# Performance work log

Hardware: AMD Instinct MI355X
Metric: run time of the kernel (lower is better)

## Reference

```python
import jax, jax.numpy as jnp
import numpy as np

D_MODEL = 512
DK = 4
DV = 8
HIDD = 10
HEAD = D_MODEL // DV  # 64
LN_EPS = 1e-5


def setup_inputs() -> dict:
    key = jax.random.key(0)
    ks = jax.random.split(key, 10)
    B, S, Se = 8, 512, 512
    u = jax.random.uniform  # torch.rand initializer for attention weights
    n = jax.random.normal
    return {
        "x": n(ks[0], (B, S, D_MODEL), jnp.float32),
        "x_enc": n(ks[1], (B, Se, D_MODEL), jnp.float32),
        "WqM": u(ks[2], (D_MODEL, HEAD * DK), jnp.float32),
        "WkM": u(ks[3], (D_MODEL, HEAD * DK), jnp.float32),
        "WvM": u(ks[4], (D_MODEL, HEAD * DV), jnp.float32),
        "ln_g": jnp.ones((D_MODEL,), jnp.float32),
        "ln_b": jnp.zeros((D_MODEL,), jnp.float32),
        "fc1_w": n(ks[5], (HIDD, D_MODEL), jnp.float32) * (1.0 / np.sqrt(D_MODEL)),
        "fc1_b": jnp.zeros((HIDD,), jnp.float32),
        "fc2_w": n(ks[6], (D_MODEL, HIDD), jnp.float32) * (1.0 / np.sqrt(HIDD)),
        "fc2_b": jnp.zeros((D_MODEL,), jnp.float32),
    }


def _attention(Xq, Xkv, WqM, WkM, WvM, causal_mul_mask):
    # NOTE: cross-attention in the source also uses WqM/WkM/WvM (Wq/Wk/Wv unused).
    B, Sq, _ = Xq.shape
    Sk = Xkv.shape[1]
    Q = (Xq @ WqM).reshape(B, Sq, HEAD, DK)
    K = (Xkv @ WkM).reshape(B, Sk, HEAD, DK)
    V = (Xkv @ WvM).reshape(B, Sk, HEAD, DV)
    score = jnp.einsum('bqhd,bkhd->bhqk', Q, K) / np.sqrt(DK).astype(np.float32)
    if causal_mul_mask:
        # Faithful quirk: multiplicative tril mask on scores (NOT additive -inf).
        score = score * jnp.tril(jnp.ones((Sq, Sk), score.dtype))
    w = jax.nn.softmax(score, axis=-1)
    out = jnp.einsum('bhqk,bkhd->bqhd', w, V)
    return out.reshape(B, Sq, HEAD * DV)  # HEAD*DV == d_model


def _layernorm(x, g, b):
    mu = jnp.mean(x, axis=-1, keepdims=True)
    var = jnp.mean(jnp.square(x - mu), axis=-1, keepdims=True)
    return (x - mu) * jax.lax.rsqrt(var + LN_EPS) * g + b


def reference(x, x_enc, WqM, WkM, WvM, ln_g, ln_b, fc1_w, fc1_b, fc2_w, fc2_b):
    fx = _attention(x, x, WqM, WkM, WvM, causal_mul_mask=True)
    fx = _attention(fx, x_enc, WqM, WkM, WvM, causal_mul_mask=False)
    y = _layernorm(x + fx, ln_g, ln_b)
    h = jax.nn.relu(y @ fc1_w.T + fc1_b)
    return h @ fc2_w.T + fc2_b
```

## Files before the change

### kernel.cpp

```cpp
#include <hip/hip_runtime.h>
#include <math.h>

#define D_MODEL 512
#define BATCH 8
#define SEQ 512
#define HEAD 64
#define DK 4
#define DV 8
#define HIDD 10

#define MR 32
#define KC 32
#define NC 256

__global__ __launch_bounds__(256) void proj_kernel(
    const float* __restrict__ xq, const float* __restrict__ xkv,
    const float* __restrict__ Wq, const float* __restrict__ Wk,
    const float* __restrict__ Wv,
    float* __restrict__ Q2, float* __restrict__ K2, float* __restrict__ V2)
{
    __shared__ float xt[KC * MR];
    __shared__ float wt[KC * NC];

    const int t  = threadIdx.x;
    const int bj = blockIdx.x & 3;
    const int br = blockIdx.x >> 2;
    const int r0 = br * MR;

    const float* X; const float* W; int ldw; int c0;
    if (bj == 0)      { X = xq;  W = Wq; ldw = 256; c0 = 0;   }
    else if (bj == 1) { X = xkv; W = Wk; ldw = 256; c0 = 0;   }
    else if (bj == 2) { X = xkv; W = Wv; ldw = 512; c0 = 0;   }
    else              { X = xkv; W = Wv; ldw = 512; c0 = 256; }

    const int rg = t >> 6;
    const int cq = t & 63;
    const int rs = t & 31;
    const int kq = t >> 5;

    float4 acc[8];
#pragma unroll
    for (int r = 0; r < 8; ++r) acc[r] = make_float4(0.f, 0.f, 0.f, 0.f);

    for (int kc = 0; kc < D_MODEL; kc += KC) {
        const float4 xa = *(const float4*)(X + (long)(r0 + rs) * D_MODEL + kc + kq * 4);
        xt[(kq * 4 + 0) * MR + rs] = xa.x;
        xt[(kq * 4 + 1) * MR + rs] = xa.y;
        xt[(kq * 4 + 2) * MR + rs] = xa.z;
        xt[(kq * 4 + 3) * MR + rs] = xa.w;

#pragma unroll
        for (int i = 0; i < 8; ++i) {
            const int row = i * 4 + rg;
            *(float4*)(wt + row * NC + cq * 4) =
                *(const float4*)(W + (long)(kc + row) * ldw + c0 + cq * 4);
        }
        __syncthreads();

#pragma unroll 4
        for (int k = 0; k < KC; ++k) {
            const float4 w4 = *(const float4*)(wt + k * NC + cq * 4);
            const float4 x0 = *(const float4*)(xt + k * MR + rg * 8);
            const float4 x1 = *(const float4*)(xt + k * MR + rg * 8 + 4);
            const float xr[8] = {x0.x, x0.y, x0.z, x0.w, x1.x, x1.y, x1.z, x1.w};
#pragma unroll
            for (int r = 0; r < 8; ++r) {
                acc[r].x = fmaf(xr[r], w4.x, acc[r].x);
                acc[r].y = fmaf(xr[r], w4.y, acc[r].y);
                acc[r].z = fmaf(xr[r], w4.z, acc[r].z);
                acc[r].w = fmaf(xr[r], w4.w, acc[r].w);
            }
        }
        __syncthreads();
    }

    const int b = r0 >> 9;
    const int sb = (r0 & 511) + rg * 8;
    if (bj <= 1) {
        float* dst = (bj == 0) ? Q2 : K2;
#pragma unroll
        for (int r = 0; r < 8; ++r)
            *(float4*)(dst + (((long)b * HEAD + cq) * SEQ + sb + r) * 4) = acc[r];
    } else {
        const int col = c0 + cq * 4;
        const int h = col >> 3;
        const int off = col & 7;
#pragma unroll
        for (int r = 0; r < 8; ++r)
            *(float4*)(V2 + (((long)b * HEAD + h) * SEQ + sb + r) * 8 + off) = acc[r];
    }
}

__global__ __launch_bounds__(256) void attn_kernel(
    const float* __restrict__ Q2, const float* __restrict__ K2,
    const float* __restrict__ V2, float* __restrict__ O, int causal)
{
    extern __shared__ float smem[];
    float* Kl = smem;
    float* Vl = smem + SEQ * DK;
    float* cs = Vl + SEQ * DV;

    const int t = threadIdx.x;
    const int bh = blockIdx.x >> 1;
    const int qhalf = blockIdx.x & 1;
    const int b = bh >> 6;
    const int h = bh & 63;

    const float4* Ks = (const float4*)(K2 + (long)bh * SEQ * DK);
    ((float4*)Kl)[t]       = Ks[t];
    ((float4*)Kl)[t + 256] = Ks[t + 256];
    const float4* Vs = (const float4*)(V2 + (long)bh * SEQ * DV);
#pragma unroll
    for (int i = 0; i < 4; ++i)
        ((float4*)Vl)[t + i * 256] = Vs[t + i * 256];
    __syncthreads();

    if (causal) {
        const int ch = t >> 3, d = t & 7;
        float s16 = 0.f;
#pragma unroll
        for (int i = 0; i < 16; ++i) s16 += Vl[(ch * 16 + i) * 8 + d];
        cs[ch * 8 + d] = s16;
        __syncthreads();
        if (t < 8) {
            cs[256 + t] = 0.f;
            float run = 0.f;
            for (int c2 = 31; c2 >= 0; --c2) {
                run += cs[c2 * 8 + t];
                cs[c2 * 8 + t] = run;
            }
        }
        __syncthreads();
    }

    const int q = qhalf * 256 + t;
    const float4 qv = *(const float4*)(Q2 + ((long)bh * SEQ + q) * 4);
    const float q0 = qv.x * 0.5f, q1 = qv.y * 0.5f;
    const float q2 = qv.z * 0.5f, q3 = qv.w * 0.5f;

    const int bound = causal ? q : (SEQ - 1);

    float m = -INFINITY, l = 0.f;
    float a0=0.f,a1=0.f,a2=0.f,a3=0.f,a4=0.f,a5=0.f,a6=0.f,a7=0.f;

    int s0 = 0;
    for (; s0 + 8 <= bound + 1; s0 += 8) {
        float sc[8];
#pragma unroll
        for (int i = 0; i < 8; ++i) {
            const float4 k4 = *(const float4*)(Kl + (s0 + i) * 4);
            sc[i] = fmaf(q0, k4.x, fmaf(q1, k4.y, fmaf(q2, k4.z, q3 * k4.w)));
        }
        float gm = fmaxf(fmaxf(fmaxf(sc[0], sc[1]), fmaxf(sc[2], sc[3])),
                         fmaxf(fmaxf(sc[4], sc[5]), fmaxf(sc[6], sc[7])));
        if (gm > m) {
            float scale = __expf(m - gm);
            l *= scale;
            a0*=scale; a1*=scale; a2*=scale; a3*=scale;
            a4*=scale; a5*=scale; a6*=scale; a7*=scale;
            m = gm;
        }
#pragma unroll
        for (int i = 0; i < 8; ++i) {
            float p = __expf(sc[i] - m);
            l += p;
            const float4 v0 = *(const float4*)(Vl + (s0 + i) * 8);
            const float4 v1 = *(const float4*)(Vl + (s0 + i) * 8 + 4);
            a0 = fmaf(p, v0.x, a0); a1 = fmaf(p, v0.y, a1);
            a2 = fmaf(p, v0.z, a2); a3 = fmaf(p, v0.w, a3);
            a4 = fmaf(p, v1.x, a4); a5 = fmaf(p, v1.y, a5);
            a6 = fmaf(p, v1.z, a6); a7 = fmaf(p, v1.w, a7);
        }
    }
    for (int s = s0; s <= bound; ++s) {
        const float4 k4 = *(const float4*)(Kl + s * 4);
        float sc = fmaf(q0, k4.x, fmaf(q1, k4.y, fmaf(q2, k4.z, q3 * k4.w)));
        if (sc > m) {
            float scale = __expf(m - sc);
            l *= scale;
            a0*=scale; a1*=scale; a2*=scale; a3*=scale;
            a4*=scale; a5*=scale; a6*=scale; a7*=scale;
            m = sc;
        }
        float p = __expf(sc - m);
        l += p;
        const float4 v0 = *(const float4*)(Vl + s * 8);
        const float4 v1 = *(const float4*)(Vl + s * 8 + 4);
        a0 = fmaf(p, v0.x, a0); a1 = fmaf(p, v0.y, a1);
        a2 = fmaf(p, v0.z, a2); a3 = fmaf(p, v0.w, a3);
        a4 = fmaf(p, v1.x, a4); a5 = fmaf(p, v1.y, a5);
        a6 = fmaf(p, v1.z, a6); a7 = fmaf(p, v1.w, a7);
    }

    if (causal && q < SEQ - 1) {
        float M = fmaxf(m, 0.f);
        float scale = __expf(m - M);
        float pm = __expf(-M);
        l = l * scale + pm * (float)(SEQ - 1 - q);
        int nq = q + 1;
        int cq2 = nq >> 4;
        float sv[8];
#pragma unroll
        for (int d = 0; d < 8; ++d) sv[d] = cs[(cq2 + 1) * 8 + d];
        for (int s = nq; s < (cq2 + 1) * 16; ++s) {
            const float4 v0 = *(const float4*)(Vl + s * 8);
            const float4 v1 = *(const float4*)(Vl + s * 8 + 4);
            sv[0]+=v0.x; sv[1]+=v0.y; sv[2]+=v0.z; sv[3]+=v0.w;
            sv[4]+=v1.x; sv[5]+=v1.y; sv[6]+=v1.z; sv[7]+=v1.w;
        }
        a0 = a0*scale + pm*sv[0]; a1 = a1*scale + pm*sv[1];
        a2 = a2*scale + pm*sv[2]; a3 = a3*scale + pm*sv[3];
        a4 = a4*scale + pm*sv[4]; a5 = a5*scale + pm*sv[5];
        a6 = a6*scale + pm*sv[6]; a7 = a7*scale + pm*sv[7];
    }

    float inv = 1.0f / l;
    const long obase = (long)b * SEQ * 512 + (long)q * 512 + h * DV;
    *(float4*)(O + obase)     = make_float4(a0*inv, a1*inv, a2*inv, a3*inv);
    *(float4*)(O + obase + 4) = make_float4(a4*inv, a5*inv, a6*inv, a7*inv);
}

__global__ __launch_bounds__(256) void ln_mlp_kernel(
    const float* __restrict__ x, const float* __restrict__ fx,
    const float* __restrict__ g, const float* __restrict__ beta,
    const float* __restrict__ w1, const float* __restrict__ b1,
    const float* __restrict__ w2, const float* __restrict__ b2,
    float* __restrict__ out)
{
    const int t = threadIdx.x;
    const int lane = t & 63;
    const int row = blockIdx.x * 4 + (t >> 6);
    const long base = (long)row * D_MODEL;
    const int e0 = lane * 8;

    const float4 xa = *(const float4*)(x + base + e0);
    const float4 xb = *(const float4*)(x + base + e0 + 4);
    const float4 fa = *(const float4*)(fx + base + e0);
    const float4 fb = *(const float4*)(fx + base + e0 + 4);
    float z[8] = {xa.x+fa.x, xa.y+fa.y, xa.z+fa.z, xa.w+fa.w,
                  xb.x+fb.x, xb.y+fb.y, xb.z+fb.z, xb.w+fb.w};

    float sum = 0.f;
#pragma unroll
    for (int j = 0; j < 8; ++j) sum += z[j];
#pragma unroll
    for (int o = 32; o > 0; o >>= 1) sum += __shfl_xor(sum, o);
    float mu = sum * (1.0f / 512.0f);

    float d[8], ss = 0.f;
#pragma unroll
    for (int j = 0; j < 8; ++j) { d[j] = z[j] - mu; ss += d[j] * d[j]; }
#pragma unroll
    for (int o = 32; o > 0; o >>= 1) ss += __shfl_xor(ss, o);
    float rs = rsqrtf(ss * (1.0f / 512.0f) + 1e-5f);

    const float4 ga = *(const float4*)(g + e0);
    const float4 gb = *(const float4*)(g + e0 + 4);
    const float4 ba = *(const float4*)(beta + e0);
    const float4 bb = *(const float4*)(beta + e0 + 4);
    const float gg[8] = {ga.x,ga.y,ga.z,ga.w,gb.x,gb.y,gb.z,gb.w};
    const float bt[8] = {ba.x,ba.y,ba.z,ba.w,bb.x,bb.y,bb.z,bb.w};
    float y[8];
#pragma unroll
    for (int j = 0; j < 8; ++j) y[j] = d[j] * rs * gg[j] + bt[j];

    float part[HIDD];
#pragma unroll
    for (int i = 0; i < HIDD; ++i) {
        const float4 wa = *(const float4*)(w1 + i * 512 + e0);
        const float4 wb = *(const float4*)(w1 + i * 512 + e0 + 4);
        part[i] = y[0]*wa.x + y[1]*wa.y + y[2]*wa.z + y[3]*wa.w
                + y[4]*wb.x + y[5]*wb.y + y[6]*wb.z + y[7]*wb.w;
    }
#pragma unroll
    for (int i = 0; i < HIDD; ++i)
#pragma unroll
        for (int o = 32; o > 0; o >>= 1) part[i] += __shfl_xor(part[i], o);

    float hv[HIDD];
#pragma unroll
    for (int i = 0; i < HIDD; ++i) hv[i] = fmaxf(part[i] + b1[i], 0.f);

    float o8[8];
#pragma unroll
    for (int j = 0; j < 8; ++j) o8[j] = b2[e0 + j];
#pragma unroll
    for (int i = 0; i < HIDD; ++i)
#pragma unroll
        for (int j = 0; j < 8; ++j)
            o8[j] = fmaf(hv[i], w2[(long)(e0 + j) * 10 + i], o8[j]);

    *(float4*)(out + base + e0)     = make_float4(o8[0], o8[1], o8[2], o8[3]);
    *(float4*)(out + base + e0 + 4) = make_float4(o8[4], o8[5], o8[6], o8[7]);
}

extern "C" void kernel_launch(void* const* d_in, const int* in_sizes, int n_in,
                              void* d_out, int out_size, void* d_ws, size_t ws_size,
                              hipStream_t stream) {
    (void)in_sizes; (void)n_in; (void)out_size; (void)ws_size;
    const float* x    = (const float*)d_in[0];
    const float* xenc = (const float*)d_in[1];
    const float* Wq   = (const float*)d_in[2];
    const float* Wk   = (const float*)d_in[3];
    const float* Wv   = (const float*)d_in[4];
    const float* ln_g = (const float*)d_in[5];
    const float* ln_b = (const float*)d_in[6];
    const float* w1   = (const float*)d_in[7];
    const float* b1   = (const float*)d_in[8];
    const float* w2   = (const float*)d_in[9];
    const float* b2   = (const float*)d_in[10];
    float* out = (float*)d_out;

    float* ws = (float*)d_ws;
    float* Q2 = ws;
    float* K2 = Q2 + 1048576;
    float* V2 = K2 + 1048576;
    float* A  = V2 + 2097152;

    const int nrows = BATCH * SEQ;
    const size_t lds_cross  = (size_t)(SEQ * DK + SEQ * DV) * 4;
    const size_t lds_causal = lds_cross + (size_t)(33 * DV) * 4;
    const int proj_grid = (nrows / MR) * 4;

    proj_kernel<<<dim3(proj_grid), 256, 0, stream>>>(x, x, Wq, Wk, Wv, Q2, K2, V2);
    attn_kernel<<<dim3(BATCH * HEAD * 2), 256, lds_causal, stream>>>(Q2, K2, V2, A, 1);

    proj_kernel<<<dim3(proj_grid), 256, 0, stream>>>(A, xenc, Wq, Wk, Wv, Q2, K2, V2);
    attn_kernel<<<dim3(BATCH * HEAD * 2), 256, lds_cross, stream>>>(Q2, K2, V2, A, 0);

    ln_mlp_kernel<<<dim3(nrows / 4), 256, 0, stream>>>(x, A, ln_g, ln_b,
                                                       w1, b1, w2, b2, out);
}
```

Measured before the change: 340.8 us.

## Enlarge projection register tile and process two queries per attention thread

The projection GEMM now uses 64-row tiles with an 8x8 register tile per thread, which raises arithmetic intensity per LDS load. The attention kernel handles two interleaved queries per thread, launches one block per (batch, head) instead of two, and turns the causal flag into a template parameter. Interleaving the queries also balances the causal work within each block. The risks are higher register pressure and half as many attention blocks, which lowers occupancy and parallelism.

```diff
diff --git a/kernel.cpp b/kernel.cpp
--- a/kernel.cpp
+++ b/kernel.cpp
@@ -9,7 +9,7 @@
 #define DV 8
 #define HIDD 10
 
-#define MR 32
+#define MR 64
 #define KC 32
 #define NC 256
 
@@ -33,22 +33,32 @@
     else if (bj == 2) { X = xkv; W = Wv; ldw = 512; c0 = 0;   }
     else              { X = xkv; W = Wv; ldw = 512; c0 = 256; }
 
+    const int ct = t & 31;
+    const int rt = t >> 5;
+    const int rs = t & 63;
+    const int kx = t >> 6;
     const int rg = t >> 6;
     const int cq = t & 63;
-    const int rs = t & 31;
-    const int kq = t >> 5;
-
-    float4 acc[8];
-#pragma unroll
-    for (int r = 0; r < 8; ++r) acc[r] = make_float4(0.f, 0.f, 0.f, 0.f);
+
+    float acc[8][8];
+#pragma unroll
+    for (int r = 0; r < 8; ++r)
+#pragma unroll
+        for (int c = 0; c < 8; ++c) acc[r][c] = 0.f;
 
     for (int kc = 0; kc < D_MODEL; kc += KC) {
-        const float4 xa = *(const float4*)(X + (long)(r0 + rs) * D_MODEL + kc + kq * 4);
-        xt[(kq * 4 + 0) * MR + rs] = xa.x;
-        xt[(kq * 4 + 1) * MR + rs] = xa.y;
-        xt[(kq * 4 + 2) * MR + rs] = xa.z;
-        xt[(kq * 4 + 3) * MR + rs] = xa.w;
-
+        {
+            const float4 xa = *(const float4*)(X + (long)(r0 + rs) * D_MODEL + kc + kx * 8);
+            const float4 xb = *(const float4*)(X + (long)(r0 + rs) * D_MODEL + kc + kx * 8 + 4);
+            xt[(kx * 8 + 0) * MR + rs] = xa.x;
+            xt[(kx * 8 + 1) * MR + rs] = xa.y;
+            xt[(kx * 8 + 2) * MR + rs] = xa.z;
+            xt[(kx * 8 + 3) * MR + rs] = xa.w;
+            xt[(kx * 8 + 4) * MR + rs] = xb.x;
+            xt[(kx * 8 + 5) * MR + rs] = xb.y;
+            xt[(kx * 8 + 6) * MR + rs] = xb.z;
+            xt[(kx * 8 + 7) * MR + rs] = xb.w;
+        }
 #pragma unroll
         for (int i = 0; i < 8; ++i) {
             const int row = i * 4 + rg;
@@ -57,43 +67,52 @@
         }
         __syncthreads();
 
-#pragma unroll 4
+#pragma unroll 2
         for (int k = 0; k < KC; ++k) {
-            const float4 w4 = *(const float4*)(wt + k * NC + cq * 4);
-            const float4 x0 = *(const float4*)(xt + k * MR + rg * 8);
-            const float4 x1 = *(const float4*)(xt + k * MR + rg * 8 + 4);
+            const float4 w0 = *(const float4*)(wt + k * NC + ct * 8);
+            const float4 w1 = *(const float4*)(wt + k * NC + ct * 8 + 4);
+            const float4 x0 = *(const float4*)(xt + k * MR + rt * 8);
+            const float4 x1 = *(const float4*)(xt + k * MR + rt * 8 + 4);
             const float xr[8] = {x0.x, x0.y, x0.z, x0.w, x1.x, x1.y, x1.z, x1.w};
-#pragma unroll
-            for (int r = 0; r < 8; ++r) {
-                acc[r].x = fmaf(xr[r], w4.x, acc[r].x);
-                acc[r].y = fmaf(xr[r], w4.y, acc[r].y);
-                acc[r].z = fmaf(xr[r], w4.z, acc[r].z);
-                acc[r].w = fmaf(xr[r], w4.w, acc[r].w);
-            }
+            const float wc[8] = {w0.x, w0.y, w0.z, w0.w, w1.x, w1.y, w1.z, w1.w};
+#pragma unroll
+            for (int r = 0; r < 8; ++r)
+#pragma unroll
+                for (int c = 0; c < 8; ++c)
+                    acc[r][c] = fmaf(xr[r], wc[c], acc[r][c]);
         }
         __syncthreads();
     }
 
-    const int b = r0 >> 9;
-    const int sb = (r0 & 511) + rg * 8;
+    const int b  = r0 >> 9;
+    const int sb = (r0 & 511) + rt * 8;
     if (bj <= 1) {
         float* dst = (bj == 0) ? Q2 : K2;
-#pragma unroll
-        for (int r = 0; r < 8; ++r)
-            *(float4*)(dst + (((long)b * HEAD + cq) * SEQ + sb + r) * 4) = acc[r];
+        const long h0 = (long)b * HEAD + ct * 2;
+#pragma unroll
+        for (int r = 0; r < 8; ++r) {
+            *(float4*)(dst + (h0 * SEQ + sb + r) * 4) =
+                make_float4(acc[r][0], acc[r][1], acc[r][2], acc[r][3]);
+            *(float4*)(dst + ((h0 + 1) * SEQ + sb + r) * 4) =
+                make_float4(acc[r][4], acc[r][5], acc[r][6], acc[r][7]);
+        }
     } else {
-        const int col = c0 + cq * 4;
-        const int h = col >> 3;
-        const int off = col & 7;
-#pragma unroll
-        for (int r = 0; r < 8; ++r)
-            *(float4*)(V2 + (((long)b * HEAD + h) * SEQ + sb + r) * 8 + off) = acc[r];
+        const int h = (c0 >> 3) + ct;
+        const long vb = ((long)b * HEAD + h) * SEQ;
+#pragma unroll
+        for (int r = 0; r < 8; ++r) {
+            *(float4*)(V2 + (vb + sb + r) * 8) =
+                make_float4(acc[r][0], acc[r][1], acc[r][2], acc[r][3]);
+            *(float4*)(V2 + (vb + sb + r) * 8 + 4) =
+                make_float4(acc[r][4], acc[r][5], acc[r][6], acc[r][7]);
+        }
     }
 }
 
+template <int CAUSAL>
 __global__ __launch_bounds__(256) void attn_kernel(
     const float* __restrict__ Q2, const float* __restrict__ K2,
-    const float* __restrict__ V2, float* __restrict__ O, int causal)
+    const float* __restrict__ V2, float* __restrict__ O)
 {
     extern __shared__ float smem[];
     float* Kl = smem;
@@ -101,8 +120,7 @@
     float* cs = Vl + SEQ * DV;
 
     const int t = threadIdx.x;
-    const int bh = blockIdx.x >> 1;
-    const int qhalf = blockIdx.x & 1;
+    const int bh = blockIdx.x;
     const int b = bh >> 6;
     const int h = bh & 63;
 
@@ -115,7 +133,7 @@
         ((float4*)Vl)[t + i * 256] = Vs[t + i * 256];
     __syncthreads();
 
-    if (causal) {
+    if (CAUSAL) {
         const int ch = t >> 3, d = t & 7;
         float s16 = 0.f;
 #pragma unroll
@@ -133,72 +151,102 @@
         __syncthreads();
     }
 
-    const int q = qhalf * 256 + t;
-    const float4 qv = *(const float4*)(Q2 + ((long)bh * SEQ + q) * 4);
-    const float q0 = qv.x * 0.5f, q1 = qv.y * 0.5f;
-    const float q2 = qv.z * 0.5f, q3 = qv.w * 0.5f;
-
-    const int bound = causal ? q : (SEQ - 1);
-
-    float m = -INFINITY, l = 0.f;
-    float a0=0.f,a1=0.f,a2=0.f,a3=0.f,a4=0.f,a5=0.f,a6=0.f,a7=0.f;
+    const int q0 = 2 * t, q1 = 2 * t + 1;
+    const float4 qa = *(const float4*)(Q2 + ((long)bh * SEQ + q0) * 4);
+    const float4 qb = *(const float4*)(Q2 + ((long)bh * SEQ + q1) * 4);
+    const float qa0 = qa.x*0.5f, qa1 = qa.y*0.5f, qa2 = qa.z*0.5f, qa3 = qa.w*0.5f;
+    const float qb0 = qb.x*0.5f, qb1 = qb.y*0.5f, qb2 = qb.z*0.5f, qb3 = qb.w*0.5f;
+
+    const int bound = CAUSAL ? q1 : (SEQ - 1);
+
+    float m0 = -INFINITY, l0 = 0.f, m1 = -INFINITY, l1 = 0.f;
+    float A0[8], A1[8];
+#pragma unroll
+    for (int d = 0; d < 8; ++d) { A0[d] = 0.f; A1[d] = 0.f; }
 
     int s0 = 0;
     for (; s0 + 8 <= bound + 1; s0 += 8) {
-        float sc[8];
+        float sa[8], sb[8];
 #pragma unroll
         for (int i = 0; i < 8; ++i) {
             const float4 k4 = *(const float4*)(Kl + (s0 + i) * 4);
-            sc[i] = fmaf(q0, k4.x, fmaf(q1, k4.y, fmaf(q2, k4.z, q3 * k4.w)));
-        }
-        float gm = fmaxf(fmaxf(fmaxf(sc[0], sc[1]), fmaxf(sc[2], sc[3])),
-                         fmaxf(fmaxf(sc[4], sc[5]), fmaxf(sc[6], sc[7])));
-        if (gm > m) {
-            float scale = __expf(m - gm);
-            l *= scale;
-            a0*=scale; a1*=scale; a2*=scale; a3*=scale;
-            a4*=scale; a5*=scale; a6*=scale; a7*=scale;
-            m = gm;
+            sa[i] = fmaf(qa0, k4.x, fmaf(qa1, k4.y, fmaf(qa2, k4.z, qa3 * k4.w)));
+            sb[i] = fmaf(qb0, k4.x, fmaf(qb1, k4.y, fmaf(qb2, k4.z, qb3 * k4.w)));
+            if (CAUSAL) sa[i] = (s0 + i <= q0) ? sa[i] : 0.f;
+        }
+        float ga = fmaxf(fmaxf(fmaxf(sa[0], sa[1]), fmaxf(sa[2], sa[3])),
+                         fmaxf(fmaxf(sa[4], sa[5]), fmaxf(sa[6], sa[7])));
+        float gb = fmaxf(fmaxf(fmaxf(sb[0], sb[1]), fmaxf(sb[2], sb[3])),
+                         fmaxf(fmaxf(sb[4], sb[5]), fmaxf(sb[6], sb[7])));
+        if (ga > m0) {
+            float sc = __expf(m0 - ga);
+            l0 *= sc;
+#pragma unroll
+            for (int d = 0; d < 8; ++d) A0[d] *= sc;
+            m0 = ga;
+        }
+        if (gb > m1) {
+            float sc = __expf(m1 - gb);
+            l1 *= sc;
+#pragma unroll
+            for (int d = 0; d < 8; ++d) A1[d] *= sc;
+            m1 = gb;
         }
 #pragma unroll
         for (int i = 0; i < 8; ++i) {
-            float p = __expf(sc[i] - m);
-            l += p;
+            float p0 = __expf(sa[i] - m0);
+            float p1 = __expf(sb[i] - m1);
+            l0 += p0; l1 += p1;
             const float4 v0 = *(const float4*)(Vl + (s0 + i) * 8);
             const float4 v1 = *(const float4*)(Vl + (s0 + i) * 8 + 4);
-            a0 = fmaf(p, v0.x, a0); a1 = fmaf(p, v0.y, a1);
-            a2 = fmaf(p, v0.z, a2); a3 = fmaf(p, v0.w, a3);
-            a4 = fmaf(p, v1.x, a4); a5 = fmaf(p, v1.y, a5);
-            a6 = fmaf(p, v1.z, a6); a7 = fmaf(p, v1.w, a7);
+            A0[0] = fmaf(p0, v0.x, A0[0]); A0[1] = fmaf(p0, v0.y, A0[1]);
+            A0[2] = fmaf(p0, v0.z, A0[2]); A0[3] = fmaf(p0, v0.w, A0[3]);
+            A0[4] = fmaf(p0, v1.x, A0[4]); A0[5] = fmaf(p0, v1.y, A0[5]);
+            A0[6] = fmaf(p0, v1.z, A0[6]); A0[7] = fmaf(p0, v1.w, A0[7]);
+            A1[0] = fmaf(p1, v0.x, A1[0]); A1[1] = fmaf(p1, v0.y, A1[1]);
+            A1[2] = fmaf(p1, v0.z, A1[2]); A1[3] = fmaf(p1, v0.w, A1[3]);
+            A1[4] = fmaf(p1, v1.x, A1[4]); A1[5] = fmaf(p1, v1.y, A1[5]);
+            A1[6] = fmaf(p1, v1.z, A1[6]); A1[7] = fmaf(p1, v1.w, A1[7]);
         }
     }
     for (int s = s0; s <= bound; ++s) {
         const float4 k4 = *(const float4*)(Kl + s * 4);
-        float sc = fmaf(q0, k4.x, fmaf(q1, k4.y, fmaf(q2, k4.z, q3 * k4.w)));
-        if (sc > m) {
-            float scale = __expf(m - sc);
-            l *= scale;
-            a0*=scale; a1*=scale; a2*=scale; a3*=scale;
-            a4*=scale; a5*=scale; a6*=scale; a7*=scale;
-            m = sc;
-        }
-        float p = __expf(sc - m);
-        l += p;
+        float sa = fmaf(qa0, k4.x, fmaf(qa1, k4.y, fmaf(qa2, k4.z, qa3 * k4.w)));
+        float sb = fmaf(qb0, k4.x, fmaf(qb1, k4.y, fmaf(qb2, k4.z, qb3 * k4.w)));
+        if (CAUSAL) sa = (s <= q0) ? sa : 0.f;
+        if (sa > m0) {
+            float sc = __expf(m0 - sa);
+            l0 *= sc;
+#pragma unroll
+            for (int d = 0; d < 8; ++d) A0[d] *= sc;
+            m0 = sa;
+        }
+        if (sb > m1) {
+            float sc = __expf(m1 - sb);
+            l1 *= sc;
+#pragma unroll
+            for (int d = 0; d < 8; ++d) A1[d] *= sc;
+            m1 = sb;
+        }
+        float p0 = __expf(sa - m0);
+        float p1 = __expf(sb - m1);
+        l0 += p0; l1 += p1;
         const float4 v0 = *(const float4*)(Vl + s * 8);
         const float4 v1 = *(const float4*)(Vl + s * 8 + 4);
-        a0 = fmaf(p, v0.x, a0); a1 = fmaf(p, v0.y, a1);
-        a2 = fmaf(p, v0.z, a2); a3 = fmaf(p, v0.w, a3);
-        a4 = fmaf(p, v1.x, a4); a5 = fmaf(p, v1.y, a5);
-        a6 = fmaf(p, v1.z, a6); a7 = fmaf(p, v1.w, a7);
-    }
-
-    if (causal && q < SEQ - 1) {
-        float M = fmaxf(m, 0.f);
-        float scale = __expf(m - M);
-        float pm = __expf(-M);
-        l = l * scale + pm * (float)(SEQ - 1 - q);
-        int nq = q + 1;
-        int cq2 = nq >> 4;
+        A0[0] = fmaf(p0, v0.x, A0[0]); A0[1] = fmaf(p0, v0.y, A0[1]);
+        A0[2] = fmaf(p0, v0.z, A0[2]); A0[3] = fmaf(p0, v0.w, A0[3]);
+        A0[4] = fmaf(p0, v1.x, A0[4]); A0[5] = fmaf(p0, v1.y, A0[5]);
+        A0[6] = fmaf(p0, v1.z, A0[6]); A0[7] = fmaf(p0, v1.w, A0[7]);
+        A1[0] = fmaf(p1, v0.x, A1[0]); A1[1] = fmaf(p1, v0.y, A1[1]);
+        A1[2] = fmaf(p1, v0.z, A1[2]); A1[3] = fmaf(p1, v0.w, A1[3]);
+        A1[4] = fmaf(p1, v1.x, A1[4]); A1[5] = fmaf(p1, v1.y, A1[5]);
+        A1[6] = fmaf(p1, v1.z, A1[6]); A1[7] = fmaf(p1, v1.w, A1[7]);
+    }
+
+    if (CAUSAL && t < 255) {
+        const int n = SEQ - 1 - q1;
+        const int nq = q1 + 1;
+        const int cq2 = nq >> 4;
         float sv[8];
 #pragma unroll
         for (int d = 0; d < 8; ++d) sv[d] = cs[(cq2 + 1) * 8 + d];
@@ -208,16 +256,26 @@
             sv[0]+=v0.x; sv[1]+=v0.y; sv[2]+=v0.z; sv[3]+=v0.w;
             sv[4]+=v1.x; sv[5]+=v1.y; sv[6]+=v1.z; sv[7]+=v1.w;
         }
-        a0 = a0*scale + pm*sv[0]; a1 = a1*scale + pm*sv[1];
-        a2 = a2*scale + pm*sv[2]; a3 = a3*scale + pm*sv[3];
-        a4 = a4*scale + pm*sv[4]; a5 = a5*scale + pm*sv[5];
-        a6 = a6*scale + pm*sv[6]; a7 = a7*scale + pm*sv[7];
-    }
-
-    float inv = 1.0f / l;
-    const long obase = (long)b * SEQ * 512 + (long)q * 512 + h * DV;
-    *(float4*)(O + obase)     = make_float4(a0*inv, a1*inv, a2*inv, a3*inv);
-    *(float4*)(O + obase + 4) = make_float4(a4*inv, a5*inv, a6*inv, a7*inv);
+        float pm0 = __expf(-m0);
+        l0 += pm0 * (float)n;
+#pragma unroll
+        for (int d = 0; d < 8; ++d) A0[d] = fmaf(pm0, sv[d], A0[d]);
+
+        float M1 = fmaxf(m1, 0.f);
+        float sc1 = __expf(m1 - M1);
+        float pm1 = __expf(-M1);
+        l1 = l1 * sc1 + pm1 * (float)n;
+#pragma unroll
+        for (int d = 0; d < 8; ++d) A1[d] = A1[d] * sc1 + pm1 * sv[d];
+    }
+
+    const float i0 = 1.0f / l0, i1 = 1.0f / l1;
+    const long ob0 = ((long)b * SEQ + q0) * 512 + h * DV;
+    const long ob1 = ((long)b * SEQ + q1) * 512 + h * DV;
+    *(float4*)(O + ob0)     = make_float4(A0[0]*i0, A0[1]*i0, A0[2]*i0, A0[3]*i0);
+    *(float4*)(O + ob0 + 4) = make_float4(A0[4]*i0, A0[5]*i0, A0[6]*i0, A0[7]*i0);
+    *(float4*)(O + ob1)     = make_float4(A1[0]*i1, A1[1]*i1, A1[2]*i1, A1[3]*i1);
+    *(float4*)(O + ob1 + 4) = make_float4(A1[4]*i1, A1[5]*i1, A1[6]*i1, A1[7]*i1);
 }
 
 __global__ __launch_bounds__(256) void ln_mlp_kernel(
@@ -323,10 +381,10 @@
     const int proj_grid = (nrows / MR) * 4;
 
     proj_kernel<<<dim3(proj_grid), 256, 0, stream>>>(x, x, Wq, Wk, Wv, Q2, K2, V2);
-    attn_kernel<<<dim3(BATCH * HEAD * 2), 256, lds_causal, stream>>>(Q2, K2, V2, A, 1);
+    attn_kernel<1><<<dim3(BATCH * HEAD), 256, lds_causal, stream>>>(Q2, K2, V2, A);
 
     proj_kernel<<<dim3(proj_grid), 256, 0, stream>>>(A, xenc, Wq, Wk, Wv, Q2, K2, V2);
-    attn_kernel<<<dim3(BATCH * HEAD * 2), 256, lds_cross, stream>>>(Q2, K2, V2, A, 0);
+    attn_kernel<0><<<dim3(BATCH * HEAD), 256, lds_cross, stream>>>(Q2, K2, V2, A);
 
     ln_mlp_kernel<<<dim3(nrows / 4), 256, 0, stream>>>(x, A, ln_g, ln_b,
                                                        w1, b1, w2, b2, out);
```

New measurement: 403.6 us. +18.4%, slower.

## Enlarge projection tiles with register prefetch and batch four queries per attention thread

Applied to the files above, without the earlier changes.

The projection GEMM doubles its row tile to 64 and gives each thread two column groups. It also prefetches the next K-chunk of X and W into registers while the current chunk is computed, so global loads overlap with FMAs. The attention kernel becomes a template on causality and runs one 128-thread block per (batch, head), with each thread owning four consecutive queries so every K/V value read from LDS is reused four times. In exchange, the grids become smaller (fewer waves to hide latency) and register pressure rises, which could lower occupancy on the GPU.

```diff
diff --git a/kernel.cpp b/kernel.cpp
--- a/kernel.cpp
+++ b/kernel.cpp
@@ -9,7 +9,7 @@
 #define DV 8
 #define HIDD 10
 
-#define MR 32
+#define MR 64
 #define KC 32
 #define NC 256
 
@@ -33,67 +33,109 @@
     else if (bj == 2) { X = xkv; W = Wv; ldw = 512; c0 = 0;   }
     else              { X = xkv; W = Wv; ldw = 512; c0 = 256; }
 
-    const int rg = t >> 6;
-    const int cq = t & 63;
-    const int rs = t & 31;
-    const int kq = t >> 5;
-
-    float4 acc[8];
-#pragma unroll
-    for (int r = 0; r < 8; ++r) acc[r] = make_float4(0.f, 0.f, 0.f, 0.f);
+    const int ct   = t & 31;
+    const int rt   = t >> 5;
+    const int rs   = t & 63;
+    const int kx   = t >> 6;
+    const int lane = t & 63;
+    const int wv   = t >> 6;
+
+    float4 accL[8], accH[8];
+#pragma unroll
+    for (int r = 0; r < 8; ++r) {
+        accL[r] = make_float4(0.f, 0.f, 0.f, 0.f);
+        accH[r] = make_float4(0.f, 0.f, 0.f, 0.f);
+    }
+
+    float4 px0, px1, pw[8];
+    {
+        const float* xb = X + (long)(r0 + rs) * D_MODEL + 0 + kx * 8;
+        px0 = *(const float4*)(xb);
+        px1 = *(const float4*)(xb + 4);
+#pragma unroll
+        for (int i = 0; i < 8; ++i) {
+            const int row = i * 4 + wv;
+            pw[i] = *(const float4*)(W + (long)(0 + row) * ldw + c0 + lane * 4);
+        }
+    }
 
     for (int kc = 0; kc < D_MODEL; kc += KC) {
-        const float4 xa = *(const float4*)(X + (long)(r0 + rs) * D_MODEL + kc + kq * 4);
-        xt[(kq * 4 + 0) * MR + rs] = xa.x;
-        xt[(kq * 4 + 1) * MR + rs] = xa.y;
-        xt[(kq * 4 + 2) * MR + rs] = xa.z;
-        xt[(kq * 4 + 3) * MR + rs] = xa.w;
-
-#pragma unroll
-        for (int i = 0; i < 8; ++i) {
-            const int row = i * 4 + rg;
-            *(float4*)(wt + row * NC + cq * 4) =
-                *(const float4*)(W + (long)(kc + row) * ldw + c0 + cq * 4);
-        }
         __syncthreads();
-
-#pragma unroll 4
+        xt[(kx * 8 + 0) * MR + rs] = px0.x;
+        xt[(kx * 8 + 1) * MR + rs] = px0.y;
+        xt[(kx * 8 + 2) * MR + rs] = px0.z;
+        xt[(kx * 8 + 3) * MR + rs] = px0.w;
+        xt[(kx * 8 + 4) * MR + rs] = px1.x;
+        xt[(kx * 8 + 5) * MR + rs] = px1.y;
+        xt[(kx * 8 + 6) * MR + rs] = px1.z;
+        xt[(kx * 8 + 7) * MR + rs] = px1.w;
+#pragma unroll
+        for (int i = 0; i < 8; ++i)
+            *(float4*)(wt + (i * 4 + wv) * NC + lane * 4) = pw[i];
+        __syncthreads();
+
+        const int kn = kc + KC;
+        if (kn < D_MODEL) {
+            const float* xb = X + (long)(r0 + rs) * D_MODEL + kn + kx * 8;
+            px0 = *(const float4*)(xb);
+            px1 = *(const float4*)(xb + 4);
+#pragma unroll
+            for (int i = 0; i < 8; ++i) {
+                const int row = i * 4 + wv;
+                pw[i] = *(const float4*)(W + (long)(kn + row) * ldw + c0 + lane * 4);
+            }
+        }
+
+#pragma unroll 2
         for (int k = 0; k < KC; ++k) {
-            const float4 w4 = *(const float4*)(wt + k * NC + cq * 4);
-            const float4 x0 = *(const float4*)(xt + k * MR + rg * 8);
-            const float4 x1 = *(const float4*)(xt + k * MR + rg * 8 + 4);
+            const float4 w0 = *(const float4*)(wt + k * NC + ct * 4);
+            const float4 w1 = *(const float4*)(wt + k * NC + 128 + ct * 4);
+            const float4 x0 = *(const float4*)(xt + k * MR + rt * 8);
+            const float4 x1 = *(const float4*)(xt + k * MR + rt * 8 + 4);
             const float xr[8] = {x0.x, x0.y, x0.z, x0.w, x1.x, x1.y, x1.z, x1.w};
 #pragma unroll
             for (int r = 0; r < 8; ++r) {
-                acc[r].x = fmaf(xr[r], w4.x, acc[r].x);
-                acc[r].y = fmaf(xr[r], w4.y, acc[r].y);
-                acc[r].z = fmaf(xr[r], w4.z, acc[r].z);
-                acc[r].w = fmaf(xr[r], w4.w, acc[r].w);
-            }
-        }
-        __syncthreads();
-    }
-
-    const int b = r0 >> 9;
-    const int sb = (r0 & 511) + rg * 8;
+                accL[r].x = fmaf(xr[r], w0.x, accL[r].x);
+                accL[r].y = fmaf(xr[r], w0.y, accL[r].y);
+                accL[r].z = fmaf(xr[r], w0.z, accL[r].z);
+                accL[r].w = fmaf(xr[r], w0.w, accL[r].w);
+                accH[r].x = fmaf(xr[r], w1.x, accH[r].x);
+                accH[r].y = fmaf(xr[r], w1.y, accH[r].y);
+                accH[r].z = fmaf(xr[r], w1.z, accH[r].z);
+                accH[r].w = fmaf(xr[r], w1.w, accH[r].w);
+            }
+        }
+    }
+
+    const int b  = r0 >> 9;
+    const int sb = (r0 & 511) + rt * 8;
     if (bj <= 1) {
         float* dst = (bj == 0) ? Q2 : K2;
-#pragma unroll
-        for (int r = 0; r < 8; ++r)
-            *(float4*)(dst + (((long)b * HEAD + cq) * SEQ + sb + r) * 4) = acc[r];
+        const long hlo = ((long)b * HEAD + ct) * SEQ;
+        const long hhi = ((long)b * HEAD + 32 + ct) * SEQ;
+#pragma unroll
+        for (int r = 0; r < 8; ++r) {
+            *(float4*)(dst + (hlo + sb + r) * 4) = accL[r];
+            *(float4*)(dst + (hhi + sb + r) * 4) = accH[r];
+        }
     } else {
-        const int col = c0 + cq * 4;
-        const int h = col >> 3;
-        const int off = col & 7;
-#pragma unroll
-        for (int r = 0; r < 8; ++r)
-            *(float4*)(V2 + (((long)b * HEAD + h) * SEQ + sb + r) * 8 + off) = acc[r];
+        const int clo = c0 + ct * 4;
+        const int chi = clo + 128;
+        const long vlo = ((long)b * HEAD + (clo >> 3)) * SEQ;
+        const long vhi = ((long)b * HEAD + (chi >> 3)) * SEQ;
+        const int off = (ct & 1) * 4;
+#pragma unroll
+        for (int r = 0; r < 8; ++r) {
+            *(float4*)(V2 + (vlo + sb + r) * 8 + off) = accL[r];
+            *(float4*)(V2 + (vhi + sb + r) * 8 + off) = accH[r];
+        }
     }
 }
 
-__global__ __launch_bounds__(256) void attn_kernel(
+template <int CAUSAL>
+__global__ __launch_bounds__(128) void attn_kernel(
     const float* __restrict__ Q2, const float* __restrict__ K2,
-    const float* __restrict__ V2, float* __restrict__ O, int causal)
+    const float* __restrict__ V2, float* __restrict__ O)
 {
     extern __shared__ float smem[];
     float* Kl = smem;
@@ -101,26 +143,27 @@
     float* cs = Vl + SEQ * DV;
 
     const int t = threadIdx.x;
-    const int bh = blockIdx.x >> 1;
-    const int qhalf = blockIdx.x & 1;
+    const int bh = blockIdx.x;
     const int b = bh >> 6;
     const int h = bh & 63;
 
     const float4* Ks = (const float4*)(K2 + (long)bh * SEQ * DK);
-    ((float4*)Kl)[t]       = Ks[t];
-    ((float4*)Kl)[t + 256] = Ks[t + 256];
+#pragma unroll
+    for (int i = 0; i < 4; ++i) ((float4*)Kl)[t + i * 128] = Ks[t + i * 128];
     const float4* Vs = (const float4*)(V2 + (long)bh * SEQ * DV);
 #pragma unroll
-    for (int i = 0; i < 4; ++i)
-        ((float4*)Vl)[t + i * 256] = Vs[t + i * 256];
+    for (int i = 0; i < 8; ++i) ((float4*)Vl)[t + i * 128] = Vs[t + i * 128];
     __syncthreads();
 
-    if (causal) {
-        const int ch = t >> 3, d = t & 7;
-        float s16 = 0.f;
-#pragma unroll
-        for (int i = 0; i < 16; ++i) s16 += Vl[(ch * 16 + i) * 8 + d];
-        cs[ch * 8 + d] = s16;
+    if (CAUSAL) {
+#pragma unroll
+        for (int w = t; w < 256; w += 128) {
+            const int ch = w >> 3, d = w & 7;
+            float s16 = 0.f;
+#pragma unroll
+            for (int i = 0; i < 16; ++i) s16 += Vl[(ch * 16 + i) * 8 + d];
+            cs[ch * 8 + d] = s16;
+        }
         __syncthreads();
         if (t < 8) {
             cs[256 + t] = 0.f;
@@ -133,91 +176,132 @@
         __syncthreads();
     }
 
-    const int q = qhalf * 256 + t;
-    const float4 qv = *(const float4*)(Q2 + ((long)bh * SEQ + q) * 4);
-    const float q0 = qv.x * 0.5f, q1 = qv.y * 0.5f;
-    const float q2 = qv.z * 0.5f, q3 = qv.w * 0.5f;
-
-    const int bound = causal ? q : (SEQ - 1);
-
-    float m = -INFINITY, l = 0.f;
-    float a0=0.f,a1=0.f,a2=0.f,a3=0.f,a4=0.f,a5=0.f,a6=0.f,a7=0.f;
+    const int qb = 4 * t;
+    float qf[4][4];
+#pragma unroll
+    for (int j = 0; j < 4; ++j) {
+        const float4 qv = *(const float4*)(Q2 + ((long)bh * SEQ + qb + j) * 4);
+        qf[j][0] = qv.x * 0.5f; qf[j][1] = qv.y * 0.5f;
+        qf[j][2] = qv.z * 0.5f; qf[j][3] = qv.w * 0.5f;
+    }
+
+    float m[4], l[4], A[4][8];
+#pragma unroll
+    for (int j = 0; j < 4; ++j) {
+        m[j] = -INFINITY; l[j] = 0.f;
+#pragma unroll
+        for (int d = 0; d < 8; ++d) A[j][d] = 0.f;
+    }
+
+    const int full_end = CAUSAL ? (qb + 1) : SEQ;
 
     int s0 = 0;
-    for (; s0 + 8 <= bound + 1; s0 += 8) {
-        float sc[8];
+    for (; s0 + 8 <= full_end; s0 += 8) {
+        float sc[4][8];
 #pragma unroll
         for (int i = 0; i < 8; ++i) {
             const float4 k4 = *(const float4*)(Kl + (s0 + i) * 4);
-            sc[i] = fmaf(q0, k4.x, fmaf(q1, k4.y, fmaf(q2, k4.z, q3 * k4.w)));
-        }
-        float gm = fmaxf(fmaxf(fmaxf(sc[0], sc[1]), fmaxf(sc[2], sc[3])),
-                         fmaxf(fmaxf(sc[4], sc[5]), fmaxf(sc[6], sc[7])));
-        if (gm > m) {
-            float scale = __expf(m - gm);
-            l *= scale;
-            a0*=scale; a1*=scale; a2*=scale; a3*=scale;
-            a4*=scale; a5*=scale; a6*=scale; a7*=scale;
-            m = gm;
+#pragma unroll
+            for (int j = 0; j < 4; ++j)
+                sc[j][i] = fmaf(qf[j][0], k4.x, fmaf(qf[j][1], k4.y,
+                           fmaf(qf[j][2], k4.z, qf[j][3] * k4.w)));
+        }
+#pragma unroll
+        for (int j = 0; j < 4; ++j) {
+            float gm = fmaxf(fmaxf(fmaxf(sc[j][0], sc[j][1]), fmaxf(sc[j][2], sc[j][3])),
+                             fmaxf(fmaxf(sc[j][4], sc[j][5]), fmaxf(sc[j][6], sc[j][7])));
+            if (gm > m[j]) {
+                const float r = __expf(m[j] - gm);
+                l[j] *= r;
+#pragma unroll
+                for (int d = 0; d < 8; ++d) A[j][d] *= r;
+                m[j] = gm;
+            }
         }
 #pragma unroll
         for (int i = 0; i < 8; ++i) {
-            float p = __expf(sc[i] - m);
-            l += p;
             const float4 v0 = *(const float4*)(Vl + (s0 + i) * 8);
             const float4 v1 = *(const float4*)(Vl + (s0 + i) * 8 + 4);
-            a0 = fmaf(p, v0.x, a0); a1 = fmaf(p, v0.y, a1);
-            a2 = fmaf(p, v0.z, a2); a3 = fmaf(p, v0.w, a3);
-            a4 = fmaf(p, v1.x, a4); a5 = fmaf(p, v1.y, a5);
-            a6 = fmaf(p, v1.z, a6); a7 = fmaf(p, v1.w, a7);
-        }
-    }
-    for (int s = s0; s <= bound; ++s) {
-        const float4 k4 = *(const float4*)(Kl + s * 4);
-        float sc = fmaf(q0, k4.x, fmaf(q1, k4.y, fmaf(q2, k4.z, q3 * k4.w)));
-        if (sc > m) {
-            float scale = __expf(m - sc);
-            l *= scale;
-            a0*=scale; a1*=scale; a2*=scale; a3*=scale;
-            a4*=scale; a5*=scale; a6*=scale; a7*=scale;
-            m = sc;
-        }
-        float p = __expf(sc - m);
-        l += p;
-        const float4 v0 = *(const float4*)(Vl + s * 8);
-        const float4 v1 = *(const float4*)(Vl + s * 8 + 4);
-        a0 = fmaf(p, v0.x, a0); a1 = fmaf(p, v0.y, a1);
-        a2 = fmaf(p, v0.z, a2); a3 = fmaf(p, v0.w, a3);
-        a4 = fmaf(p, v1.x, a4); a5 = fmaf(p, v1.y, a5);
-        a6 = fmaf(p, v1.z, a6); a7 = fmaf(p, v1.w, a7);
-    }
-
-    if (causal && q < SEQ - 1) {
-        float M = fmaxf(m, 0.f);
-        float scale = __expf(m - M);
-        float pm = __expf(-M);
-        l = l * scale + pm * (float)(SEQ - 1 - q);
-        int nq = q + 1;
-        int cq2 = nq >> 4;
-        float sv[8];
-#pragma unroll
-        for (int d = 0; d < 8; ++d) sv[d] = cs[(cq2 + 1) * 8 + d];
-        for (int s = nq; s < (cq2 + 1) * 16; ++s) {
+#pragma unroll
+            for (int j = 0; j < 4; ++j) {
+                const float p = __expf(sc[j][i] - m[j]);
+                l[j] += p;
+                A[j][0] = fmaf(p, v0.x, A[j][0]); A[j][1] = fmaf(p, v0.y, A[j][1]);
+                A[j][2] = fmaf(p, v0.z, A[j][2]); A[j][3] = fmaf(p, v0.w, A[j][3]);
+                A[j][4] = fmaf(p, v1.x, A[j][4]); A[j][5] = fmaf(p, v1.y, A[j][5]);
+                A[j][6] = fmaf(p, v1.z, A[j][6]); A[j][7] = fmaf(p, v1.w, A[j][7]);
+            }
+        }
+    }
+
+    if (CAUSAL) {
+        const int q3 = qb + 3;
+        for (int s = s0; s <= q3; ++s) {
+            const float4 k4 = *(const float4*)(Kl + s * 4);
+            float scj[4];
+#pragma unroll
+            for (int j = 0; j < 4; ++j)
+                scj[j] = fmaf(qf[j][0], k4.x, fmaf(qf[j][1], k4.y,
+                         fmaf(qf[j][2], k4.z, qf[j][3] * k4.w)));
+            scj[0] = (s <= qb)     ? scj[0] : 0.f;
+            scj[1] = (s <= qb + 1) ? scj[1] : 0.f;
+            scj[2] = (s <= qb + 2) ? scj[2] : 0.f;
             const float4 v0 = *(const float4*)(Vl + s * 8);
             const float4 v1 = *(const float4*)(Vl + s * 8 + 4);
-            sv[0]+=v0.x; sv[1]+=v0.y; sv[2]+=v0.z; sv[3]+=v0.w;
-            sv[4]+=v1.x; sv[5]+=v1.y; sv[6]+=v1.z; sv[7]+=v1.w;
-        }
-        a0 = a0*scale + pm*sv[0]; a1 = a1*scale + pm*sv[1];
-        a2 = a2*scale + pm*sv[2]; a3 = a3*scale + pm*sv[3];
-        a4 = a4*scale + pm*sv[4]; a5 = a5*scale + pm*sv[5];
-        a6 = a6*scale + pm*sv[6]; a7 = a7*scale + pm*sv[7];
-    }
-
-    float inv = 1.0f / l;
-    const long obase = (long)b * SEQ * 512 + (long)q * 512 + h * DV;
-    *(float4*)(O + obase)     = make_float4(a0*inv, a1*inv, a2*inv, a3*inv);
-    *(float4*)(O + obase + 4) = make_float4(a4*inv, a5*inv, a6*inv, a7*inv);
+#pragma unroll
+            for (int j = 0; j < 4; ++j) {
+                if (scj[j] > m[j]) {
+                    const float r = __expf(m[j] - scj[j]);
+                    l[j] *= r;
+#pragma unroll
+                    for (int d = 0; d < 8; ++d) A[j][d] *= r;
+                    m[j] = scj[j];
+                }
+                const float p = __expf(scj[j] - m[j]);
+                l[j] += p;
+                A[j][0] = fmaf(p, v0.x, A[j][0]); A[j][1] = fmaf(p, v0.y, A[j][1]);
+                A[j][2] = fmaf(p, v0.z, A[j][2]); A[j][3] = fmaf(p, v0.w, A[j][3]);
+                A[j][4] = fmaf(p, v1.x, A[j][4]); A[j][5] = fmaf(p, v1.y, A[j][5]);
+                A[j][6] = fmaf(p, v1.z, A[j][6]); A[j][7] = fmaf(p, v1.w, A[j][7]);
+            }
+        }
+
+        const int n = SEQ - 1 - q3;
+        if (n > 0) {
+            const int nq = q3 + 1;
+            const int cq2 = nq >> 4;
+            float sv[8];
+#pragma unroll
+            for (int d = 0; d < 8; ++d) sv[d] = cs[(cq2 + 1) * 8 + d];
+            for (int s = nq; s < (cq2 + 1) * 16; ++s) {
+                const float4 v0 = *(const float4*)(Vl + s * 8);
+                const float4 v1 = *(const float4*)(Vl + s * 8 + 4);
+                sv[0] += v0.x; sv[1] += v0.y; sv[2] += v0.z; sv[3] += v0.w;
+                sv[4] += v1.x; sv[5] += v1.y; sv[6] += v1.z; sv[7] += v1.w;
+            }
+#pragma unroll
+            for (int j = 0; j < 3; ++j) {
+                const float pm = __expf(-m[j]);
+                l[j] += pm * (float)n;
+#pragma unroll
+                for (int d = 0; d < 8; ++d) A[j][d] = fmaf(pm, sv[d], A[j][d]);
+            }
+            const float M3  = fmaxf(m[3], 0.f);
+            const float r3  = __expf(m[3] - M3);
+            const float pm3 = __expf(-M3);
+            l[3] = l[3] * r3 + pm3 * (float)n;
+#pragma unroll
+            for (int d = 0; d < 8; ++d) A[3][d] = A[3][d] * r3 + pm3 * sv[d];
+        }
+    }
+
+#pragma unroll
+    for (int j = 0; j < 4; ++j) {
+        const float inv = 1.0f / l[j];
+        const long ob = ((long)b * SEQ + qb + j) * 512 + h * DV;
+        *(float4*)(O + ob)     = make_float4(A[j][0]*inv, A[j][1]*inv, A[j][2]*inv, A[j][3]*inv);
+        *(float4*)(O + ob + 4) = make_float4(A[j][4]*inv, A[j][5]*inv, A[j][6]*inv, A[j][7]*inv);
+    }
 }
 
 __global__ __launch_bounds__(256) void ln_mlp_kernel(
@@ -323,10 +407,10 @@
     const int proj_grid = (nrows / MR) * 4;
 
     proj_kernel<<<dim3(proj_grid), 256, 0, stream>>>(x, x, Wq, Wk, Wv, Q2, K2, V2);
-    attn_kernel<<<dim3(BATCH * HEAD * 2), 256, lds_causal, stream>>>(Q2, K2, V2, A, 1);
+    attn_kernel<1><<<dim3(BATCH * HEAD), 128, lds_causal, stream>>>(Q2, K2, V2, A);
 
     proj_kernel<<<dim3(proj_grid), 256, 0, stream>>>(A, xenc, Wq, Wk, Wv, Q2, K2, V2);
-    attn_kernel<<<dim3(BATCH * HEAD * 2), 256, lds_cross, stream>>>(Q2, K2, V2, A, 0);
+    attn_kernel<0><<<dim3(BATCH * HEAD), 128, lds_cross, stream>>>(Q2, K2, V2, A);
 
     ln_mlp_kernel<<<dim3(nrows / 4), 256, 0, stream>>>(x, A, ln_g, ln_b,
                                                        w1, b1, w2, b2, out);
```

Measured after the change: 473.5 us. 38.9% more time.
